# Optimization experiments

Measured on AMD Instinct MI355X. Metric: run time of the kernel, lower is better.

## Reference

```python
import jax, jax.numpy as jnp
import numpy as np

INV_SQRT2 = 0.7071067811865476


def setup_inputs() -> dict:
    key = jax.random.key(0)
    ks = jax.random.split(key, 10)
    B, P, MU = 65536, 2048, 7
    return {
        "dnn_out": jax.random.normal(ks[0], (B, P), jnp.float32),
        "b": jax.random.normal(ks[1], (B,), jnp.float32),
        "h": jax.random.normal(ks[2], (B,), jnp.float32),
        "x_real": jax.random.normal(ks[3], (B, 1), jnp.float32),
        "x_imag": jax.random.normal(ks[4], (B, 1), jnp.float32),
        "ISI_symbols_real": jax.random.normal(ks[5], (B, MU - 1), jnp.float32),
        "ISI_symbols_imag": jax.random.normal(ks[6], (B, MU - 1), jnp.float32),
        "ISI_channels": jax.random.normal(ks[7], (B, MU - 1), jnp.float32),
        "noise": jax.random.normal(ks[8], (B, 1), jnp.float32),
        "prob": jax.random.uniform(ks[9], (1, P), jnp.float32),
        "mu": MU,
        "num_points": P,
        "batch_size": B,
    }


def reference(dnn_out, b, h, x_real, x_imag, ISI_symbols_real, ISI_symbols_imag,
              ISI_channels, noise, prob, mu, num_points, batch_size):
    # Static loop geometry (matches np.floor in the torch code)
    mid = num_points // 2
    T = (num_points // mu) // 2
    num_ISI = mu // 2
    dists = np.arange(-T, T)                                   # [2T] outer dist loop
    w2 = np.array([w for w in range(mu) if w != num_ISI])      # inner mu loop, skip center tap
    offs = (w2 - num_ISI) * 2 * T                              # [mu-1] dnn_out column offsets
    idx = mid + dists[:, None] + offs[None, :]                 # [2T, mu-1]

    # NOTE: in the source, `index` is never incremented, so ALL ISI terms use
    # column 0 of ISI_channels / ISI_symbols. The coefficient is therefore
    # independent of w2 and the w2-sum factors out of the dnn_out gather.
    S = dnn_out[:, idx].sum(-1)                                # [B, 2T] sum over ISI taps

    b1 = b.reshape(-1, 1)                                      # torch reshape (batch,1)
    h1 = h.reshape(-1, 1)
    d0 = dnn_out[:, mid + dists]                               # [B, 2T] center-tap sample

    # A[i,d] = y_rec + noise/sqrt(2) - target  (the j-independent part)
    A_r = b1 * h1 * x_real * d0 + INV_SQRT2 * noise - x_real   # [B, 2T]
    A_i = b1 * h1 * x_imag * d0 + INV_SQRT2 * noise - x_imag

    # torch broadcasting makes y_ISI a [B,B] matrix: entry (i,j) uses
    # b[i]*dnn_out[i,.] and ISI_channels[j,0]*ISI_symbols[j,0]. The mean over
    # the [B,B] matrix of (A_i + b_i*c_j*S_i)^2 is expanded analytically over j
    # to avoid materializing [B,B]: E_j[.] = A^2 + 2*A*bS*E[c] + (bS)^2*E[c^2].
    c_r = ISI_channels[:, 0] * ISI_symbols_real[:, 0]          # [B]
    c_i = ISI_channels[:, 0] * ISI_symbols_imag[:, 0]
    m1r, m2r = jnp.mean(c_r), jnp.mean(c_r ** 2)
    m1i, m2i = jnp.mean(c_i), jnp.mean(c_i ** 2)
    bS = b1 * S                                                # [B, 2T]

    mse_r = jnp.mean(A_r ** 2 + 2.0 * A_r * bS * m1r + bS ** 2 * m2r, axis=0)  # [2T]
    mse_i = jnp.mean(A_i ** 2 + 2.0 * A_i * bS * m1i + bS ** 2 * m2i, axis=0)

    return jnp.sum(prob[0, mid + dists] * (mse_r + mse_i))
```

## Files before the change

### kernel.cpp

```cpp
#include <hip/hip_runtime.h>

#define INV_SQRT2 0.7071067811865476f

typedef float f32x4 __attribute__((ext_vector_type(4)));

__global__ __launch_bounds__(320) void isi_main_fast(
    const float* __restrict__ dnn,
    const float* __restrict__ b,
    const float* __restrict__ h,
    const float* __restrict__ xr,
    const float* __restrict__ xi,
    const float* __restrict__ sym_r,
    const float* __restrict__ sym_i,
    const float* __restrict__ chan,
    const float* __restrict__ noise,
    const float* __restrict__ prob,
    float* __restrict__ ws,
    int B, int rowsPerBlock)
{
    constexpr int P = 2048, D = 292, cbase = 2, midT = 878;

    const int tid = threadIdx.x;
    float a0 = 0.f, a1 = 0.f, a2 = 0.f, a3 = 0.f;
    float m0 = 0.f, m1 = 0.f, m2 = 0.f, m3 = 0.f;

    {
        const int gid = blockIdx.x * 320 + tid;
        const int tot = gridDim.x * 320;
        for (int i = gid; i < B; i += tot) {
            const float ch = chan[(size_t)i * 6];
            const float cr = ch * sym_r[(size_t)i * 6];
            const float ci = ch * sym_i[(size_t)i * 6];
            m0 += cr; m1 += cr * cr; m2 += ci; m3 += ci * ci;
        }
    }

    const int g  = tid / 80;
    const int jv = tid % 80;
    const bool act = (jv < 73);
    const int  j0  = 4 * jv;

    f32x4 pj = (f32x4)(0.f);
    if (act) pj = *(const f32x4*)(prob + midT + j0);

    const int row0 = blockIdx.x * rowsPerBlock;

#pragma unroll 2
    for (int r = 0; r < rowsPerBlock; r += 4) {
        const int row = row0 + r + g;
        const float* __restrict__ rp = dnn + (size_t)row * P + cbase + j0;

        const float bb  = b[row];
        const float bh  = bb * h[row];
        const float vxr = xr[row];
        const float vxi = xi[row];
        const float nz  = INV_SQRT2 * noise[row];
        const float cr0 = bh * vxr, ar_c = nz - vxr;
        const float ci0 = bh * vxi, ai_c = nz - vxi;

        if (act) {
            const f32x4 t0 = __builtin_nontemporal_load((const f32x4*)(rp + 0 * D));
            const f32x4 t1 = __builtin_nontemporal_load((const f32x4*)(rp + 1 * D));
            const f32x4 t2 = __builtin_nontemporal_load((const f32x4*)(rp + 2 * D));
            const f32x4 d0 = __builtin_nontemporal_load((const f32x4*)(rp + 3 * D));
            const f32x4 t4 = __builtin_nontemporal_load((const f32x4*)(rp + 4 * D));
            const f32x4 t5 = __builtin_nontemporal_load((const f32x4*)(rp + 5 * D));
            const f32x4 t6 = __builtin_nontemporal_load((const f32x4*)(rp + 6 * D));

            const f32x4 S = t0 + t1 + t2 + t4 + t5 + t6;

#pragma unroll
            for (int c = 0; c < 4; ++c) {
                const float Ar = cr0 * d0[c] + ar_c;
                const float Ai = ci0 * d0[c] + ai_c;
                const float bS = bb * S[c];
                const float p  = pj[c];
                a0 += p * (Ar * Ar + Ai * Ai);
                a1 += p * (Ar * bS);
                a2 += p * (Ai * bS);
                a3 += p * (bS * bS);
            }
        }
    }

    __shared__ float red[8][5];
    float v[8] = {a0, a1, a2, a3, m0, m1, m2, m3};
    const int wave = tid >> 6, lane = tid & 63;
#pragma unroll
    for (int s = 0; s < 8; ++s) {
        float x = v[s];
#pragma unroll
        for (int off = 32; off > 0; off >>= 1) x += __shfl_down(x, off, 64);
        if (lane == 0) red[s][wave] = x;
    }
    __syncthreads();
    if (tid < 8) {
        float x = red[tid][0] + red[tid][1] + red[tid][2]
                + red[tid][3] + red[tid][4];
        ws[(size_t)blockIdx.x * 8 + tid] = x;
    }
}

__global__ __launch_bounds__(256) void isi_main_generic(
    const float* __restrict__ dnn,
    const float* __restrict__ b,
    const float* __restrict__ h,
    const float* __restrict__ xr,
    const float* __restrict__ xi,
    const float* __restrict__ sym_r,
    const float* __restrict__ sym_i,
    const float* __restrict__ chan,
    const float* __restrict__ noise,
    const float* __restrict__ prob,
    float* __restrict__ ws,
    int B, int P, int D, int MU, int cbase, int midT, int rowsPerBlock)
{
    const int tid = threadIdx.x;
    float a0 = 0.f, a1 = 0.f, a2 = 0.f, a3 = 0.f;
    float m0 = 0.f, m1 = 0.f, m2 = 0.f, m3 = 0.f;
    const int st = MU - 1;
    {
        const int gid = blockIdx.x * 256 + tid;
        const int tot = gridDim.x * 256;
        for (int i = gid; i < B; i += tot) {
            const float ch = chan[(size_t)i * st];
            const float cr = ch * sym_r[(size_t)i * st];
            const float ci = ch * sym_i[(size_t)i * st];
            m0 += cr; m1 += cr * cr; m2 += ci; m3 += ci * ci;
        }
    }
    const int row0 = blockIdx.x * rowsPerBlock;
    const int row1 = min(B, row0 + rowsPerBlock);
    const int nISI = MU / 2;

    for (int row = row0; row < row1; ++row) {
        const float* __restrict__ rp = dnn + (size_t)row * P;
        const float bb  = b[row];
        const float bh  = bb * h[row];
        const float vxr = xr[row];
        const float vxi = xi[row];
        const float nz  = INV_SQRT2 * noise[row];
        const float cr0 = bh * vxr, ar_c = nz - vxr;
        const float ci0 = bh * vxi, ai_c = nz - vxi;
        for (int j = tid; j < D; j += 256) {
            float sum7 = 0.f, d0 = 0.f;
            for (int k = 0; k < MU; ++k) {
                const float t = rp[cbase + k * D + j];
                sum7 += t;
                if (k == nISI) d0 = t;
            }
            const float S  = sum7 - d0;
            const float Ar = cr0 * d0 + ar_c;
            const float Ai = ci0 * d0 + ai_c;
            const float bS = bb * S;
            const float pj = prob[midT + j];
            a0 += pj * (Ar * Ar + Ai * Ai);
            a1 += pj * (Ar * bS);
            a2 += pj * (Ai * bS);
            a3 += pj * (bS * bS);
        }
    }

    __shared__ float red[8][4];
    float v[8] = {a0, a1, a2, a3, m0, m1, m2, m3};
    const int wave = tid >> 6, lane = tid & 63;
#pragma unroll
    for (int s = 0; s < 8; ++s) {
        float x = v[s];
#pragma unroll
        for (int off = 32; off > 0; off >>= 1) x += __shfl_down(x, off, 64);
        if (lane == 0) red[s][wave] = x;
    }
    __syncthreads();
    if (tid < 8) {
        float x = red[tid][0] + red[tid][1] + red[tid][2] + red[tid][3];
        ws[(size_t)blockIdx.x * 8 + tid] = x;
    }
}

__global__ void isi_final(const float* __restrict__ ws,
                          float* __restrict__ out, int nblk, int B)
{
    const int lane = threadIdx.x;
    float v[8] = {0.f, 0.f, 0.f, 0.f, 0.f, 0.f, 0.f, 0.f};
    for (int i = lane; i < nblk; i += 64) {
        const float* p = ws + (size_t)i * 8;
#pragma unroll
        for (int s = 0; s < 8; ++s) v[s] += p[s];
    }
#pragma unroll
    for (int s = 0; s < 8; ++s) {
        float x = v[s];
#pragma unroll
        for (int off = 32; off > 0; off >>= 1) x += __shfl_down(x, off, 64);
        v[s] = x;
    }
    if (lane == 0) {
        const float invB = 1.0f / (float)B;
        const float P0 = v[0], P1r = v[1], P1i = v[2], P2 = v[3];
        const float m1r = v[4] * invB, m2r = v[5] * invB;
        const float m1i = v[6] * invB, m2i = v[7] * invB;
        out[0] = (P0 + 2.0f * (m1r * P1r + m1i * P1i)
                  + (m2r + m2i) * P2) * invB;
    }
}

extern "C" void kernel_launch(void* const* d_in, const int* in_sizes, int n_in,
                              void* d_out, int out_size, void* d_ws, size_t ws_size,
                              hipStream_t stream)
{
    const float* dnn   = (const float*)d_in[0];
    const float* b     = (const float*)d_in[1];
    const float* h     = (const float*)d_in[2];
    const float* xr    = (const float*)d_in[3];
    const float* xi    = (const float*)d_in[4];
    const float* sym_r = (const float*)d_in[5];
    const float* sym_i = (const float*)d_in[6];
    const float* chan  = (const float*)d_in[7];
    const float* noise = (const float*)d_in[8];
    const float* prob  = (const float*)d_in[9];

    const int B  = in_sizes[1];
    const int P  = in_sizes[0] / B;
    const int MU = in_sizes[5] / B + 1;

    const int T     = (P / MU) / 2;
    const int D     = 2 * T;
    const int mid   = P / 2;
    const int midT  = mid - T;
    const int cbase = midT - (MU / 2) * D;

    const int rowsPerBlock = 16;
    const int grid = (B + rowsPerBlock - 1) / rowsPerBlock;

    if (P == 2048 && MU == 7 && D == 292 && cbase == 2 && midT == 878 &&
        (B % rowsPerBlock) == 0) {
        isi_main_fast<<<grid, 320, 0, stream>>>(
            dnn, b, h, xr, xi, sym_r, sym_i, chan, noise, prob,
            (float*)d_ws, B, rowsPerBlock);
    } else {
        isi_main_generic<<<grid, 256, 0, stream>>>(
            dnn, b, h, xr, xi, sym_r, sym_i, chan, noise, prob,
            (float*)d_ws, B, P, D, MU, cbase, midT, rowsPerBlock);
    }
    isi_final<<<1, 64, 0, stream>>>((const float*)d_ws, (float*)d_out, grid, B);
}
```

Baseline: 687.0 us.

## Stage dnn rows into LDS via global_load_lds and halve rows per block

```diff
diff --git a/kernel.cpp b/kernel.cpp
--- a/kernel.cpp
+++ b/kernel.cpp
@@ -3,6 +3,14 @@
 #define INV_SQRT2 0.7071067811865476f
 
 typedef float f32x4 __attribute__((ext_vector_type(4)));
+
+__device__ __forceinline__ void stage16(const float* g, float* l)
+{
+    __builtin_amdgcn_global_load_lds(
+        (const __attribute__((address_space(1))) void*)g,
+        (__attribute__((address_space(3))) void*)l,
+        16, 0, 0);
+}
 
 __global__ __launch_bounds__(320) void isi_main_fast(
     const float* __restrict__ dnn,
@@ -18,7 +26,11 @@
     float* __restrict__ ws,
     int B, int rowsPerBlock)
 {
-    constexpr int P = 2048, D = 292, cbase = 2, midT = 878;
+    constexpr int P = 2048, D = 292, midT = 878;
+    constexpr int CPR = 511;
+    constexpr int CPS = 4 * CPR;
+
+    __shared__ float lds[CPS * 4];
 
     const int tid = threadIdx.x;
     float a0 = 0.f, a1 = 0.f, a2 = 0.f, a3 = 0.f;
@@ -43,13 +55,31 @@
     f32x4 pj = (f32x4)(0.f);
     if (act) pj = *(const f32x4*)(prob + midT + j0);
 
-    const int row0 = blockIdx.x * rowsPerBlock;
-
-#pragma unroll 2
+    const int row0     = blockIdx.x * rowsPerBlock;
+    const int waveBase = tid & ~63;
+
     for (int r = 0; r < rowsPerBlock; r += 4) {
+        const float* stepBase = dnn + (size_t)(row0 + r) * P;
+
+#pragma unroll
+        for (int i = 0; i < 6; ++i) {
+            const unsigned q  = (unsigned)(tid + 320 * i);
+            const unsigned gr = q / 511u;
+            const unsigned c  = q - 511u * gr;
+            stage16(stepBase + (size_t)gr * P + 2 + 4 * c,
+                    lds + 4 * (waveBase + 320 * i));
+        }
+        {
+            const unsigned q = (unsigned)(tid + 1920);
+            if (q < (unsigned)CPS) {
+                const unsigned gr = q / 511u;
+                const unsigned c  = q - 511u * gr;
+                stage16(stepBase + (size_t)gr * P + 2 + 4 * c,
+                        lds + 4 * (waveBase + 1920));
+            }
+        }
+
         const int row = row0 + r + g;
-        const float* __restrict__ rp = dnn + (size_t)row * P + cbase + j0;
-
         const float bb  = b[row];
         const float bh  = bb * h[row];
         const float vxr = xr[row];
@@ -58,14 +88,17 @@
         const float cr0 = bh * vxr, ar_c = nz - vxr;
         const float ci0 = bh * vxi, ai_c = nz - vxi;
 
+        __syncthreads();
+
         if (act) {
-            const f32x4 t0 = __builtin_nontemporal_load((const f32x4*)(rp + 0 * D));
-            const f32x4 t1 = __builtin_nontemporal_load((const f32x4*)(rp + 1 * D));
-            const f32x4 t2 = __builtin_nontemporal_load((const f32x4*)(rp + 2 * D));
-            const f32x4 d0 = __builtin_nontemporal_load((const f32x4*)(rp + 3 * D));
-            const f32x4 t4 = __builtin_nontemporal_load((const f32x4*)(rp + 4 * D));
-            const f32x4 t5 = __builtin_nontemporal_load((const f32x4*)(rp + 5 * D));
-            const f32x4 t6 = __builtin_nontemporal_load((const f32x4*)(rp + 6 * D));
+            const float* lp = lds + g * (CPR * 4) + j0;
+            const f32x4 t0 = *(const f32x4*)(lp + 0 * D);
+            const f32x4 t1 = *(const f32x4*)(lp + 1 * D);
+            const f32x4 t2 = *(const f32x4*)(lp + 2 * D);
+            const f32x4 d0 = *(const f32x4*)(lp + 3 * D);
+            const f32x4 t4 = *(const f32x4*)(lp + 4 * D);
+            const f32x4 t5 = *(const f32x4*)(lp + 5 * D);
+            const f32x4 t6 = *(const f32x4*)(lp + 6 * D);
 
             const f32x4 S = t0 + t1 + t2 + t4 + t5 + t6;
 
@@ -81,9 +114,10 @@
                 a3 += p * (bS * bS);
             }
         }
-    }
-
-    __shared__ float red[8][5];
+        __syncthreads();
+    }
+
+    float* red = lds;
     float v[8] = {a0, a1, a2, a3, m0, m1, m2, m3};
     const int wave = tid >> 6, lane = tid & 63;
 #pragma unroll
@@ -91,12 +125,12 @@
         float x = v[s];
 #pragma unroll
         for (int off = 32; off > 0; off >>= 1) x += __shfl_down(x, off, 64);
-        if (lane == 0) red[s][wave] = x;
+        if (lane == 0) red[s * 5 + wave] = x;
     }
     __syncthreads();
     if (tid < 8) {
-        float x = red[tid][0] + red[tid][1] + red[tid][2]
-                + red[tid][3] + red[tid][4];
+        float x = red[tid * 5 + 0] + red[tid * 5 + 1] + red[tid * 5 + 2]
+                + red[tid * 5 + 3] + red[tid * 5 + 4];
         ws[(size_t)blockIdx.x * 8 + tid] = x;
     }
 }
@@ -230,18 +264,20 @@
     const int midT  = mid - T;
     const int cbase = midT - (MU / 2) * D;
 
-    const int rowsPerBlock = 16;
-    const int grid = (B + rowsPerBlock - 1) / rowsPerBlock;
-
     if (P == 2048 && MU == 7 && D == 292 && cbase == 2 && midT == 878 &&
-        (B % rowsPerBlock) == 0) {
+        (B % 8) == 0) {
+        const int rowsPerBlock = 8;
+        const int grid = B / rowsPerBlock;
         isi_main_fast<<<grid, 320, 0, stream>>>(
             dnn, b, h, xr, xi, sym_r, sym_i, chan, noise, prob,
             (float*)d_ws, B, rowsPerBlock);
+        isi_final<<<1, 64, 0, stream>>>((const float*)d_ws, (float*)d_out, grid, B);
     } else {
+        const int rowsPerBlock = 16;
+        const int grid = (B + rowsPerBlock - 1) / rowsPerBlock;
         isi_main_generic<<<grid, 256, 0, stream>>>(
             dnn, b, h, xr, xi, sym_r, sym_i, chan, noise, prob,
             (float*)d_ws, B, P, D, MU, cbase, midT, rowsPerBlock);
-    }
-    isi_final<<<1, 64, 0, stream>>>((const float*)d_ws, (float*)d_out, grid, B);
-}
+        isi_final<<<1, 64, 0, stream>>>((const float*)d_ws, (float*)d_out, grid, B);
+    }
+}
```

After: 739.7 us. +7.7%, slower.
